# Kernel optimization log

Measured on AMD Instinct MI355X. Metric: run time of the kernel, lower is better.

The kernel has to match this reference:

```python
import jax, jax.numpy as jnp
from jax import lax
import numpy as np

B, C, H, W, D = 8, 128, 96, 96, 4  # D must equal 64//16 = 4 (one UAG per depth slice)


def setup_inputs() -> dict:
    key = jax.random.key(0)
    ks = jax.random.split(key, 9)
    s = 0.5 / np.sqrt(C)  # keep the recurrence numerically stable
    def w(k):
        return jax.random.normal(k, (D, C, C), jnp.float32) * s
    def b(k):
        return jax.random.normal(k, (D, C), jnp.float32) * 0.01
    return {
        "x": jax.random.normal(ks[0], (B, C, H, W, D), jnp.float32),
        "W1": w(ks[1]), "b1": b(ks[2]),  # conv1 per-dag weights/bias (kernel_size=1 -> [C,C])
        "W2": w(ks[3]), "b2": b(ks[4]),  # conv2
        "W4": w(ks[5]), "b4": b(ks[6]),  # conv4
        "W5": w(ks[7]), "b5": b(ks[8]),  # conv5
    }


def _dag(xs, w1, bb1, w2, bb2, w4, bb4, w5, bb5):
    # xs: [B,C,H,W]; one UAG_RNN_4Neigh forward.
    def lin(w, bb, v):  # 1x1 Conv1d == channel matmul; v: [B,C,L]
        return jnp.einsum('oc,bcl->bol', w, v) + bb[None, :, None]

    # --- row recurrence (top -> bottom); row 0 passes through unchanged ---
    def row_step(prev, row):
        new = jax.nn.relu(lin(w1, bb1, row) + lin(w2, bb2, prev))
        return new, new

    row0 = xs[:, :, 0, :]                       # [B,C,W]
    rows = jnp.moveaxis(xs[:, :, 1:, :], 2, 0)  # [H-1,B,C,W]
    _, out_rows = lax.scan(row_step, row0, rows)
    hs = jnp.concatenate([row0[None], out_rows], axis=0)  # [H,B,C,W]
    hs = jnp.moveaxis(hs, 0, 2)                            # [B,C,H,W]

    # --- col recurrence (left -> right); col 0 gets relu only ---
    def col_step(prev, col):
        new = jax.nn.relu(lin(w4, bb4, col) + lin(w5, bb5, prev))
        return new, new

    col0 = jax.nn.relu(hs[:, :, :, 0])           # [B,C,H]
    cols = jnp.moveaxis(hs[:, :, :, 1:], 3, 0)   # [W-1,B,C,H]
    _, out_cols = lax.scan(col_step, col0, cols)
    hse = jnp.concatenate([col0[None], out_cols], axis=0)  # [W,B,C,H]
    return jnp.moveaxis(hse, 0, 3)                           # [B,C,H,W]


def reference(x, W1, b1, W2, b2, W4, b4, W5, b5):
    # vmap over the D=4 depth slices, each with its own dag parameters
    hid = jax.vmap(_dag, in_axes=(-1, 0, 0, 0, 0, 0, 0, 0, 0), out_axes=-1)(
        x, W1, b1, W2, b2, W4, b4, W5, b5)
    return x + hid
```

## Files before the change

kernel.cpp:

```cpp
#include <hip/hip_runtime.h>


typedef short bf16x8 __attribute__((ext_vector_type(8)));
typedef short short4v __attribute__((ext_vector_type(4)));
typedef float f32x4 __attribute__((ext_vector_type(4)));

__device__ __forceinline__ unsigned short f2bf(float f) {
  unsigned int u = __builtin_bit_cast(unsigned int, f);
  u = (u + 0x7FFFu + ((u >> 16) & 1u)) >> 16;
  return (unsigned short)u;
}
__device__ __forceinline__ float bf2f(unsigned short h) {
  unsigned int u = ((unsigned int)h) << 16;
  return __builtin_bit_cast(float, u);
}

#define LDS_BARRIER() asm volatile("s_waitcnt lgkmcnt(0)\n\ts_barrier" ::: "memory")

__global__ __launch_bounds__(256) void prep_kernel(
    const float* __restrict__ W1, const float* __restrict__ b1,
    const float* __restrict__ W2, const float* __restrict__ b2,
    const float* __restrict__ W4, const float* __restrict__ b4,
    const float* __restrict__ W5, const float* __restrict__ b5,
    unsigned short* __restrict__ Wb, float* __restrict__ bs12,
    float* __restrict__ bs45) {
  int gid = blockIdx.x * 256 + threadIdx.x;
  if (gid < 4 * 65536) {
    int m = gid >> 16;
    int r = gid & 65535;
    const float* src = (m == 0) ? W1 : (m == 1) ? W2 : (m == 2) ? W4 : W5;
    Wb[m * 65536 + r] = f2bf(src[r]);
  } else if (gid < 4 * 65536 + 512) {
    int r = gid - 4 * 65536;
    bs12[r] = b1[r] + b2[r];
  } else if (gid < 4 * 65536 + 1024) {
    int r = gid - 4 * 65536 - 512;
    bs45[r] = b4[r] + b5[r];
  }
}

__global__ __launch_bounds__(256) void transpose_kernel(
    const float* __restrict__ x, unsigned short* __restrict__ xT) {
  __shared__ unsigned short tile[128 * 208];
  int bid = blockIdx.x;
  int half = bid & 1;
  int rest = bid >> 1;
  int h = rest % 96;
  int b = rest / 96;
  int wd0 = half * 192;
  int tid = threadIdx.x;
#pragma unroll
  for (int it = 0; it < 12; ++it) {
    int cid = it * 256 + tid;
    int c = cid / 24;
    int k = cid % 24;
    const float* xp = x + ((size_t)(b * 128 + c) * 96 + h) * 384 + wd0 + k * 8;
    float4 v0 = *(const float4*)xp;
    float4 v1 = *(const float4*)(xp + 4);
    bf16x8 pk;
    pk[0] = (short)f2bf(v0.x); pk[1] = (short)f2bf(v0.y);
    pk[2] = (short)f2bf(v0.z); pk[3] = (short)f2bf(v0.w);
    pk[4] = (short)f2bf(v1.x); pk[5] = (short)f2bf(v1.y);
    pk[6] = (short)f2bf(v1.z); pk[7] = (short)f2bf(v1.w);
    int ks = k ^ ((c >> 3) & 7);
    *(bf16x8*)&tile[c * 208 + ks * 8] = pk;
  }
  __syncthreads();
#pragma unroll
  for (int it = 0; it < 12; ++it) {
    int sid = it * 256 + tid;
    int wdl = sid >> 4;
    int cc = sid & 15;
    int c0 = cc * 8;
    int k = wdl >> 3, off = wdl & 7;
    bf16x8 pk;
#pragma unroll
    for (int j = 0; j < 8; ++j) {
      int c = c0 + j;
      int ks = k ^ ((c >> 3) & 7);
      pk[j] = (short)tile[c * 208 + ks * 8 + off];
    }
    int wdg = wd0 + wdl;
    int d = wdg & 3, w = wdg >> 2;
    *(bf16x8*)(xT + ((((size_t)(b * 4 + d) * 96 + h) * 96 + w) * 128 + c0)) = pk;
  }
}

__global__ __launch_bounds__(256) void row_kernel(
    const unsigned short* __restrict__ xT, unsigned short* __restrict__ hs,
    const unsigned short* __restrict__ Wb, const float* __restrict__ bs12) {
  int bid = blockIdx.x;
  int wt = bid % 6;
  int bd = bid / 6;
  int d = bd & 3;
  int w0 = wt * 16;
  int tid = threadIdx.x;
  int lane = tid & 63;
  int wave = tid >> 6;
  int quad = lane >> 4;
  int n = lane & 15;

  __shared__ unsigned short prevs[2][16 * 136];

  const unsigned short* w1p = Wb + d * 16384;
  const unsigned short* w2p = Wb + 65536 + d * 16384;

  bf16x8 A1[2][4], A2[2][4];
#pragma unroll
  for (int mi = 0; mi < 2; ++mi) {
    int c = (wave * 2 + mi) * 16 + n;
#pragma unroll
    for (int kt = 0; kt < 4; ++kt) {
      int k0 = kt * 32 + quad * 8;
      A1[mi][kt] = *(const bf16x8*)(w1p + c * 128 + k0);
      A2[mi][kt] = *(const bf16x8*)(w2p + c * 128 + k0);
    }
  }
  f32x4 bias[2];
#pragma unroll
  for (int mi = 0; mi < 2; ++mi)
#pragma unroll
    for (int r = 0; r < 4; ++r)
      bias[mi][r] = bs12[d * 128 + (wave * 2 + mi) * 16 + quad * 4 + r];

  size_t bd9216 = (size_t)bd * 9216;

  {
    int wl = tid >> 4;
    int c8 = (tid & 15) * 8;
    bf16x8 v = *(const bf16x8*)(xT + (bd9216 + (size_t)(w0 + wl)) * 128 + c8);
    *(bf16x8*)&prevs[0][wl * 136 + c8] = v;
    *(bf16x8*)(hs + (bd9216 + (size_t)(w0 + wl)) * 128 + c8) = v;
  }

  bf16x8 Bt[4], Bn[4], Bf[4];
  {
    const unsigned short* p1 = xT + (bd9216 + (size_t)1 * 96 + w0 + n) * 128;
    const unsigned short* p2 = xT + (bd9216 + (size_t)2 * 96 + w0 + n) * 128;
    const unsigned short* p3 = xT + (bd9216 + (size_t)3 * 96 + w0 + n) * 128;
#pragma unroll
    for (int kt = 0; kt < 4; ++kt) {
      int k0 = kt * 32 + quad * 8;
      Bt[kt] = *(const bf16x8*)(p1 + k0);
      Bn[kt] = *(const bf16x8*)(p2 + k0);
      Bf[kt] = *(const bf16x8*)(p3 + k0);
    }
  }
  f32x4 accA[2] = {bias[0], bias[1]};
#pragma unroll
  for (int kt = 0; kt < 4; ++kt) {
    accA[0] = __builtin_amdgcn_mfma_f32_16x16x32_bf16(A1[0][kt], Bt[kt], accA[0], 0, 0, 0);
    accA[1] = __builtin_amdgcn_mfma_f32_16x16x32_bf16(A1[1][kt], Bt[kt], accA[1], 0, 0, 0);
  }

  for (int h = 1; h < 96; ++h) {
    LDS_BARRIER();
    const unsigned short* pr = &prevs[(h - 1) & 1][n * 136];
    bf16x8 Bp[4];
#pragma unroll
    for (int kt = 0; kt < 4; ++kt)
      Bp[kt] = *(const bf16x8*)(pr + kt * 32 + quad * 8);
    f32x4 acc0 = accA[0], acc1 = accA[1];
#pragma unroll
    for (int kt = 0; kt < 4; ++kt) {
      acc0 = __builtin_amdgcn_mfma_f32_16x16x32_bf16(A2[0][kt], Bp[kt], acc0, 0, 0, 0);
      acc1 = __builtin_amdgcn_mfma_f32_16x16x32_bf16(A2[1][kt], Bp[kt], acc1, 0, 0, 0);
    }
    unsigned short* pw = &prevs[h & 1][n * 136];
    unsigned short* hrow = hs + (bd9216 + (size_t)h * 96 + w0 + n) * 128;
    short4v pk0, pk1;
#pragma unroll
    for (int r = 0; r < 4; ++r) {
      float v = acc0[r]; v = v > 0.f ? v : 0.f; pk0[r] = (short)f2bf(v);
      float u = acc1[r]; u = u > 0.f ? u : 0.f; pk1[r] = (short)f2bf(u);
    }
    int co0 = (wave * 2 + 0) * 16 + quad * 4;
    int co1 = (wave * 2 + 1) * 16 + quad * 4;
    *(short4v*)(pw + co0) = pk0;
    *(short4v*)(pw + co1) = pk1;
    *(short4v*)(hrow + co0) = pk0;
    *(short4v*)(hrow + co1) = pk1;
    accA[0] = bias[0]; accA[1] = bias[1];
#pragma unroll
    for (int kt = 0; kt < 4; ++kt) {
      accA[0] = __builtin_amdgcn_mfma_f32_16x16x32_bf16(A1[0][kt], Bn[kt], accA[0], 0, 0, 0);
      accA[1] = __builtin_amdgcn_mfma_f32_16x16x32_bf16(A1[1][kt], Bn[kt], accA[1], 0, 0, 0);
    }
    int hp = (h + 3 <= 95) ? h + 3 : 95;
    const unsigned short* pf = xT + (bd9216 + (size_t)hp * 96 + w0 + n) * 128;
#pragma unroll
    for (int kt = 0; kt < 4; ++kt) {
      Bn[kt] = Bf[kt];
      Bf[kt] = *(const bf16x8*)(pf + kt * 32 + quad * 8);
    }
  }
}

__global__ __launch_bounds__(256) void col_kernel(
    const unsigned short* __restrict__ hs, unsigned short* __restrict__ hid,
    const unsigned short* __restrict__ Wb, const float* __restrict__ bs45) {
  int bid = blockIdx.x;
  int ht = bid % 6;
  int bd = bid / 6;
  int d = bd & 3;
  int h0 = ht * 16;
  int tid = threadIdx.x;
  int lane = tid & 63;
  int wave = tid >> 6;
  int quad = lane >> 4;
  int n = lane & 15;

  __shared__ unsigned short prevs[2][16 * 136];

  const unsigned short* w4p = Wb + 2 * 65536 + d * 16384;
  const unsigned short* w5p = Wb + 3 * 65536 + d * 16384;

  bf16x8 A4[2][4], A5[2][4];
#pragma unroll
  for (int mi = 0; mi < 2; ++mi) {
    int c = (wave * 2 + mi) * 16 + n;
#pragma unroll
    for (int kt = 0; kt < 4; ++kt) {
      int k0 = kt * 32 + quad * 8;
      A4[mi][kt] = *(const bf16x8*)(w4p + c * 128 + k0);
      A5[mi][kt] = *(const bf16x8*)(w5p + c * 128 + k0);
    }
  }
  f32x4 bias[2];
#pragma unroll
  for (int mi = 0; mi < 2; ++mi)
#pragma unroll
    for (int r = 0; r < 4; ++r)
      bias[mi][r] = bs45[d * 128 + (wave * 2 + mi) * 16 + quad * 4 + r];

  size_t bd9216 = (size_t)bd * 9216;

  {
    int hl = tid >> 4;
    int c8 = (tid & 15) * 8;
    size_t base = (bd9216 + (size_t)(h0 + hl) * 96) * 128 + c8;
    bf16x8 v = *(const bf16x8*)(hs + base);
#pragma unroll
    for (int j = 0; j < 8; ++j) {
      unsigned short uv = (unsigned short)v[j];
      if (uv & 0x8000u) v[j] = 0;
    }
    *(bf16x8*)&prevs[0][hl * 136 + c8] = v;
    *(bf16x8*)(hid + base) = v;
  }

  bf16x8 Bt[4], Bn[4], Bf[4];
  {
    const unsigned short* p1 = hs + (bd9216 + (size_t)(h0 + n) * 96 + 1) * 128;
    const unsigned short* p2 = hs + (bd9216 + (size_t)(h0 + n) * 96 + 2) * 128;
    const unsigned short* p3 = hs + (bd9216 + (size_t)(h0 + n) * 96 + 3) * 128;
#pragma unroll
    for (int kt = 0; kt < 4; ++kt) {
      int k0 = kt * 32 + quad * 8;
      Bt[kt] = *(const bf16x8*)(p1 + k0);
      Bn[kt] = *(const bf16x8*)(p2 + k0);
      Bf[kt] = *(const bf16x8*)(p3 + k0);
    }
  }
  f32x4 accA[2] = {bias[0], bias[1]};
#pragma unroll
  for (int kt = 0; kt < 4; ++kt) {
    accA[0] = __builtin_amdgcn_mfma_f32_16x16x32_bf16(A4[0][kt], Bt[kt], accA[0], 0, 0, 0);
    accA[1] = __builtin_amdgcn_mfma_f32_16x16x32_bf16(A4[1][kt], Bt[kt], accA[1], 0, 0, 0);
  }

  for (int w = 1; w < 96; ++w) {
    LDS_BARRIER();
    const unsigned short* pr = &prevs[(w - 1) & 1][n * 136];
    bf16x8 Bp[4];
#pragma unroll
    for (int kt = 0; kt < 4; ++kt)
      Bp[kt] = *(const bf16x8*)(pr + kt * 32 + quad * 8);
    f32x4 acc0 = accA[0], acc1 = accA[1];
#pragma unroll
    for (int kt = 0; kt < 4; ++kt) {
      acc0 = __builtin_amdgcn_mfma_f32_16x16x32_bf16(A5[0][kt], Bp[kt], acc0, 0, 0, 0);
      acc1 = __builtin_amdgcn_mfma_f32_16x16x32_bf16(A5[1][kt], Bp[kt], acc1, 0, 0, 0);
    }
    unsigned short* pw = &prevs[w & 1][n * 136];
    unsigned short* orow = hid + (bd9216 + (size_t)(h0 + n) * 96 + w) * 128;
    short4v pk0, pk1;
#pragma unroll
    for (int r = 0; r < 4; ++r) {
      float v = acc0[r]; v = v > 0.f ? v : 0.f; pk0[r] = (short)f2bf(v);
      float u = acc1[r]; u = u > 0.f ? u : 0.f; pk1[r] = (short)f2bf(u);
    }
    int co0 = (wave * 2 + 0) * 16 + quad * 4;
    int co1 = (wave * 2 + 1) * 16 + quad * 4;
    *(short4v*)(pw + co0) = pk0;
    *(short4v*)(pw + co1) = pk1;
    *(short4v*)(orow + co0) = pk0;
    *(short4v*)(orow + co1) = pk1;
    accA[0] = bias[0]; accA[1] = bias[1];
#pragma unroll
    for (int kt = 0; kt < 4; ++kt) {
      accA[0] = __builtin_amdgcn_mfma_f32_16x16x32_bf16(A4[0][kt], Bn[kt], accA[0], 0, 0, 0);
      accA[1] = __builtin_amdgcn_mfma_f32_16x16x32_bf16(A4[1][kt], Bn[kt], accA[1], 0, 0, 0);
    }
    int wp = (w + 3 <= 95) ? w + 3 : 95;
    const unsigned short* pf = hs + (bd9216 + (size_t)(h0 + n) * 96 + wp) * 128;
#pragma unroll
    for (int kt = 0; kt < 4; ++kt) {
      Bn[kt] = Bf[kt];
      Bf[kt] = *(const bf16x8*)(pf + kt * 32 + quad * 8);
    }
  }
}

__global__ __launch_bounds__(256) void out_kernel(
    const float* __restrict__ x, const unsigned short* __restrict__ hid,
    float* __restrict__ out) {
  __shared__ unsigned short tile[128 * 208];
  int bid = blockIdx.x;
  int half = bid & 1;
  int rest = bid >> 1;
  int h = rest % 96;
  int b = rest / 96;
  int wd0 = half * 192;
  int tid = threadIdx.x;
#pragma unroll
  for (int it = 0; it < 12; ++it) {
    int gid = it * 256 + tid;
    int wdl = gid >> 4;
    int cc = gid & 15;
    int c0 = cc * 8;
    int wdg = wd0 + wdl;
    int d = wdg & 3, w = wdg >> 2;
    bf16x8 v = *(const bf16x8*)(hid + ((((size_t)(b * 4 + d) * 96 + h) * 96 + w) * 128 + c0));
    int k = wdl >> 3, off = wdl & 7;
#pragma unroll
    for (int j = 0; j < 8; ++j) {
      int c = c0 + j;
      int ks = k ^ ((c >> 3) & 7);
      tile[c * 208 + ks * 8 + off] = (unsigned short)v[j];
    }
  }
  __syncthreads();
#pragma unroll
  for (int it = 0; it < 12; ++it) {
    int sid = it * 256 + tid;
    int c = sid / 24;
    int k = sid % 24;
    int ks = k ^ ((c >> 3) & 7);
    bf16x8 pk = *(const bf16x8*)&tile[c * 208 + ks * 8];
    size_t o = ((size_t)(b * 128 + c) * 96 + h) * 384 + wd0 + k * 8;
    float4 a0 = *(const float4*)(x + o);
    float4 a1 = *(const float4*)(x + o + 4);
    float4 r0, r1;
    r0.x = a0.x + bf2f((unsigned short)pk[0]);
    r0.y = a0.y + bf2f((unsigned short)pk[1]);
    r0.z = a0.z + bf2f((unsigned short)pk[2]);
    r0.w = a0.w + bf2f((unsigned short)pk[3]);
    r1.x = a1.x + bf2f((unsigned short)pk[4]);
    r1.y = a1.y + bf2f((unsigned short)pk[5]);
    r1.z = a1.z + bf2f((unsigned short)pk[6]);
    r1.w = a1.w + bf2f((unsigned short)pk[7]);
    *(float4*)(out + o) = r0;
    *(float4*)(out + o + 4) = r1;
  }
}

extern "C" void kernel_launch(void* const* d_in, const int* in_sizes, int n_in,
                              void* d_out, int out_size, void* d_ws, size_t ws_size,
                              hipStream_t stream) {
  (void)in_sizes; (void)n_in; (void)out_size; (void)ws_size;
  const float* x  = (const float*)d_in[0];
  const float* W1 = (const float*)d_in[1];
  const float* b1 = (const float*)d_in[2];
  const float* W2 = (const float*)d_in[3];
  const float* b2 = (const float*)d_in[4];
  const float* W4 = (const float*)d_in[5];
  const float* b4 = (const float*)d_in[6];
  const float* W5 = (const float*)d_in[7];
  const float* b5 = (const float*)d_in[8];
  float* out = (float*)d_out;

  char* ws = (char*)d_ws;
  unsigned short* Wb   = (unsigned short*)(ws);
  float* bs12          = (float*)(ws + 524288);
  float* bs45          = (float*)(ws + 526336);
  unsigned short* hs   = (unsigned short*)(ws + 528384);
  unsigned short* xT   = (unsigned short*)(ws + 76025856);
  unsigned short* hid  = xT;

  prep_kernel<<<(4 * 65536 + 1024 + 255) / 256, 256, 0, stream>>>(
      W1, b1, W2, b2, W4, b4, W5, b5, Wb, bs12, bs45);
  transpose_kernel<<<8 * 96 * 2, 256, 0, stream>>>(x, xT);
  row_kernel<<<192, 256, 0, stream>>>(xT, hs, Wb, bs12);
  col_kernel<<<192, 256, 0, stream>>>(hs, hid, Wb, bs45);
  out_kernel<<<8 * 96 * 2, 256, 0, stream>>>(x, hid, out);
}
```

Before: 493.6 us.

## Keep recurrence state in registers with a permuted channel layout in single-wave blocks

Channel order in the weights and activations is permuted so that each MFMA output fragment, once packed to bf16, is already the B operand for the next step. This lets a single wave per block hold all 128 output channels and carry the recurrent state in registers, removing the LDS round trip and barrier each step. The row and column scans now overwrite one in-place activation buffer, and bf16 conversion uses v_cvt_pk_bf16_f32 with two-step software pipelining. The cost is far fewer waves per CU (192 single-wave blocks), heavy VGPR pressure from 64 weight fragments, and a longer serial MFMA chain per wave.

```diff
diff --git a/kernel.cpp b/kernel.cpp
--- a/kernel.cpp
+++ b/kernel.cpp
@@ -2,8 +2,8 @@
 
 
 typedef short bf16x8 __attribute__((ext_vector_type(8)));
-typedef short short4v __attribute__((ext_vector_type(4)));
 typedef float f32x4 __attribute__((ext_vector_type(4)));
+typedef unsigned int uint4v __attribute__((ext_vector_type(4)));
 
 __device__ __forceinline__ unsigned short f2bf(float f) {
   unsigned int u = __builtin_bit_cast(unsigned int, f);
@@ -15,7 +15,10 @@
   return __builtin_bit_cast(float, u);
 }
 
-#define LDS_BARRIER() asm volatile("s_waitcnt lgkmcnt(0)\n\ts_barrier" ::: "memory")
+__device__ __forceinline__ int sigma_k(int kap) {
+  int kt = kap >> 5, q = (kap >> 3) & 3, j = kap & 7;
+  return kt * 32 + ((j >> 2) << 4) + q * 4 + (j & 3);
+}
 
 __global__ __launch_bounds__(256) void prep_kernel(
     const float* __restrict__ W1, const float* __restrict__ b1,
@@ -28,8 +31,10 @@
   if (gid < 4 * 65536) {
     int m = gid >> 16;
     int r = gid & 65535;
+    int kap = r & 127;
+    int c = sigma_k(kap);
     const float* src = (m == 0) ? W1 : (m == 1) ? W2 : (m == 2) ? W4 : W5;
-    Wb[m * 65536 + r] = f2bf(src[r]);
+    Wb[m * 65536 + r] = f2bf(src[(r >> 7) * 128 + c]);
   } else if (gid < 4 * 65536 + 512) {
     int r = gid - 4 * 65536;
     bs12[r] = b1[r] + b2[r];
@@ -40,7 +45,7 @@
 }
 
 __global__ __launch_bounds__(256) void transpose_kernel(
-    const float* __restrict__ x, unsigned short* __restrict__ xT) {
+    const float* __restrict__ x, unsigned short* __restrict__ act) {
   __shared__ unsigned short tile[128 * 208];
   int bid = blockIdx.x;
   int half = bid & 1;
@@ -71,249 +76,223 @@
     int sid = it * 256 + tid;
     int wdl = sid >> 4;
     int cc = sid & 15;
-    int c0 = cc * 8;
     int k = wdl >> 3, off = wdl & 7;
+    int ktq = cc >> 2, qq = cc & 3;
     bf16x8 pk;
 #pragma unroll
     for (int j = 0; j < 8; ++j) {
-      int c = c0 + j;
+      int c = ktq * 32 + ((j >> 2) << 4) + qq * 4 + (j & 3);
       int ks = k ^ ((c >> 3) & 7);
       pk[j] = (short)tile[c * 208 + ks * 8 + off];
     }
     int wdg = wd0 + wdl;
     int d = wdg & 3, w = wdg >> 2;
-    *(bf16x8*)(xT + ((((size_t)(b * 4 + d) * 96 + h) * 96 + w) * 128 + c0)) = pk;
-  }
-}
-
-__global__ __launch_bounds__(256) void row_kernel(
-    const unsigned short* __restrict__ xT, unsigned short* __restrict__ hs,
-    const unsigned short* __restrict__ Wb, const float* __restrict__ bs12) {
+    *(bf16x8*)(act + ((((size_t)(b * 4 + d) * 96 + h) * 96 + w) * 128 + cc * 8)) = pk;
+  }
+}
+
+#define SCAN_STEP(CUR, NXT, BN, PF)                                            \
+  do {                                                                         \
+    _Pragma("unroll") for (int kt = 0; kt < 4; ++kt)                           \
+      _Pragma("unroll") for (int mi = 0; mi < 8; ++mi)                         \
+        CUR[mi] = __builtin_amdgcn_mfma_f32_16x16x32_bf16(A2[mi][kt], Bp[kt],  \
+                                                          CUR[mi], 0, 0, 0);   \
+    _Pragma("unroll") for (int kt = 0; kt < 4; ++kt) {                         \
+      unsigned int u0, u1, u2, u3;                                             \
+      float a0 = fmaxf(CUR[2 * kt][0], 0.f);                                   \
+      float a1 = fmaxf(CUR[2 * kt][1], 0.f);                                   \
+      float a2 = fmaxf(CUR[2 * kt][2], 0.f);                                   \
+      float a3 = fmaxf(CUR[2 * kt][3], 0.f);                                   \
+      float c0 = fmaxf(CUR[2 * kt + 1][0], 0.f);                               \
+      float c1 = fmaxf(CUR[2 * kt + 1][1], 0.f);                               \
+      float c2 = fmaxf(CUR[2 * kt + 1][2], 0.f);                               \
+      float c3 = fmaxf(CUR[2 * kt + 1][3], 0.f);                               \
+      asm("v_cvt_pk_bf16_f32 %0, %1, %2" : "=v"(u0) : "v"(a0), "v"(a1));       \
+      asm("v_cvt_pk_bf16_f32 %0, %1, %2" : "=v"(u1) : "v"(a2), "v"(a3));       \
+      asm("v_cvt_pk_bf16_f32 %0, %1, %2" : "=v"(u2) : "v"(c0), "v"(c1));       \
+      asm("v_cvt_pk_bf16_f32 %0, %1, %2" : "=v"(u3) : "v"(c2), "v"(c3));       \
+      uint4v uu;                                                               \
+      uu[0] = u0; uu[1] = u1; uu[2] = u2; uu[3] = u3;                          \
+      Bp[kt] = __builtin_bit_cast(bf16x8, uu);                                 \
+      *(bf16x8*)(outrow + kt * 32) = Bp[kt];                                   \
+    }                                                                          \
+    _Pragma("unroll") for (int mi = 0; mi < 8; ++mi)                           \
+      NXT[mi] = __builtin_amdgcn_mfma_f32_16x16x32_bf16(A1[mi][0], BN[0],      \
+                                                        bias[mi], 0, 0, 0);    \
+    _Pragma("unroll") for (int kt = 1; kt < 4; ++kt)                           \
+      _Pragma("unroll") for (int mi = 0; mi < 8; ++mi)                         \
+        NXT[mi] = __builtin_amdgcn_mfma_f32_16x16x32_bf16(A1[mi][kt], BN[kt],  \
+                                                          NXT[mi], 0, 0, 0);   \
+    _Pragma("unroll") for (int kt = 0; kt < 4; ++kt)                           \
+      BN[kt] = *(const bf16x8*)(PF + kt * 32);                                 \
+    outrow += OUT_STRIDE;                                                      \
+  } while (0)
+
+__global__ __launch_bounds__(64, 1) void row_kernel(
+    unsigned short* act, const unsigned short* __restrict__ Wb,
+    const float* __restrict__ bs12) {
   int bid = blockIdx.x;
   int wt = bid % 6;
   int bd = bid / 6;
   int d = bd & 3;
   int w0 = wt * 16;
-  int tid = threadIdx.x;
-  int lane = tid & 63;
-  int wave = tid >> 6;
-  int quad = lane >> 4;
+  int lane = threadIdx.x & 63;
+  int q = lane >> 4;
   int n = lane & 15;
-
-  __shared__ unsigned short prevs[2][16 * 136];
 
   const unsigned short* w1p = Wb + d * 16384;
   const unsigned short* w2p = Wb + 65536 + d * 16384;
 
-  bf16x8 A1[2][4], A2[2][4];
-#pragma unroll
-  for (int mi = 0; mi < 2; ++mi) {
-    int c = (wave * 2 + mi) * 16 + n;
+  bf16x8 A1[8][4], A2[8][4];
+#pragma unroll
+  for (int mi = 0; mi < 8; ++mi) {
+    int c = mi * 16 + n;
 #pragma unroll
     for (int kt = 0; kt < 4; ++kt) {
-      int k0 = kt * 32 + quad * 8;
+      int k0 = kt * 32 + q * 8;
       A1[mi][kt] = *(const bf16x8*)(w1p + c * 128 + k0);
       A2[mi][kt] = *(const bf16x8*)(w2p + c * 128 + k0);
     }
   }
-  f32x4 bias[2];
-#pragma unroll
-  for (int mi = 0; mi < 2; ++mi)
+  f32x4 bias[8];
+#pragma unroll
+  for (int mi = 0; mi < 8; ++mi)
 #pragma unroll
     for (int r = 0; r < 4; ++r)
-      bias[mi][r] = bs12[d * 128 + (wave * 2 + mi) * 16 + quad * 4 + r];
-
-  size_t bd9216 = (size_t)bd * 9216;
-
+      bias[mi][r] = bs12[d * 128 + mi * 16 + q * 4 + r];
+
+  size_t base = ((size_t)bd * 9216 + (size_t)(w0 + n)) * 128 + q * 8;
+  const unsigned short* xrow = act + base;
+  unsigned short* outrow = act + base + 12288;
+  const int OUT_STRIDE = 12288;
+
+  bf16x8 Bp[4], Bn_[4], Bf_[4];
+#pragma unroll
+  for (int kt = 0; kt < 4; ++kt)
+    Bp[kt] = *(const bf16x8*)(xrow + kt * 32);
+
+  f32x4 accA_[8], accB_[8];
+#pragma unroll
+  for (int kt = 0; kt < 4; ++kt)
+    Bn_[kt] = *(const bf16x8*)(xrow + 12288 + kt * 32);
+#pragma unroll
+  for (int mi = 0; mi < 8; ++mi)
+    accA_[mi] = __builtin_amdgcn_mfma_f32_16x16x32_bf16(A1[mi][0], Bn_[0],
+                                                        bias[mi], 0, 0, 0);
+#pragma unroll
+  for (int kt = 1; kt < 4; ++kt)
+#pragma unroll
+    for (int mi = 0; mi < 8; ++mi)
+      accA_[mi] = __builtin_amdgcn_mfma_f32_16x16x32_bf16(A1[mi][kt], Bn_[kt],
+                                                          accA_[mi], 0, 0, 0);
+#pragma unroll
+  for (int kt = 0; kt < 4; ++kt) {
+    Bn_[kt] = *(const bf16x8*)(xrow + 2 * 12288 + kt * 32);
+    Bf_[kt] = *(const bf16x8*)(xrow + 3 * 12288 + kt * 32);
+  }
+
+#pragma unroll 1
+  for (int h = 1; h <= 93; h += 2) {
+    const unsigned short* pf1 =
+        xrow + (size_t)(h + 3 <= 95 ? h + 3 : 95) * 12288;
+    SCAN_STEP(accA_, accB_, Bn_, pf1);
+    const unsigned short* pf2 =
+        xrow + (size_t)(h + 4 <= 95 ? h + 4 : 95) * 12288;
+    SCAN_STEP(accB_, accA_, Bf_, pf2);
+  }
   {
-    int wl = tid >> 4;
-    int c8 = (tid & 15) * 8;
-    bf16x8 v = *(const bf16x8*)(xT + (bd9216 + (size_t)(w0 + wl)) * 128 + c8);
-    *(bf16x8*)&prevs[0][wl * 136 + c8] = v;
-    *(bf16x8*)(hs + (bd9216 + (size_t)(w0 + wl)) * 128 + c8) = v;
-  }
-
-  bf16x8 Bt[4], Bn[4], Bf[4];
-  {
-    const unsigned short* p1 = xT + (bd9216 + (size_t)1 * 96 + w0 + n) * 128;
-    const unsigned short* p2 = xT + (bd9216 + (size_t)2 * 96 + w0 + n) * 128;
-    const unsigned short* p3 = xT + (bd9216 + (size_t)3 * 96 + w0 + n) * 128;
-#pragma unroll
-    for (int kt = 0; kt < 4; ++kt) {
-      int k0 = kt * 32 + quad * 8;
-      Bt[kt] = *(const bf16x8*)(p1 + k0);
-      Bn[kt] = *(const bf16x8*)(p2 + k0);
-      Bf[kt] = *(const bf16x8*)(p3 + k0);
-    }
-  }
-  f32x4 accA[2] = {bias[0], bias[1]};
-#pragma unroll
-  for (int kt = 0; kt < 4; ++kt) {
-    accA[0] = __builtin_amdgcn_mfma_f32_16x16x32_bf16(A1[0][kt], Bt[kt], accA[0], 0, 0, 0);
-    accA[1] = __builtin_amdgcn_mfma_f32_16x16x32_bf16(A1[1][kt], Bt[kt], accA[1], 0, 0, 0);
-  }
-
-  for (int h = 1; h < 96; ++h) {
-    LDS_BARRIER();
-    const unsigned short* pr = &prevs[(h - 1) & 1][n * 136];
-    bf16x8 Bp[4];
-#pragma unroll
-    for (int kt = 0; kt < 4; ++kt)
-      Bp[kt] = *(const bf16x8*)(pr + kt * 32 + quad * 8);
-    f32x4 acc0 = accA[0], acc1 = accA[1];
-#pragma unroll
-    for (int kt = 0; kt < 4; ++kt) {
-      acc0 = __builtin_amdgcn_mfma_f32_16x16x32_bf16(A2[0][kt], Bp[kt], acc0, 0, 0, 0);
-      acc1 = __builtin_amdgcn_mfma_f32_16x16x32_bf16(A2[1][kt], Bp[kt], acc1, 0, 0, 0);
-    }
-    unsigned short* pw = &prevs[h & 1][n * 136];
-    unsigned short* hrow = hs + (bd9216 + (size_t)h * 96 + w0 + n) * 128;
-    short4v pk0, pk1;
-#pragma unroll
-    for (int r = 0; r < 4; ++r) {
-      float v = acc0[r]; v = v > 0.f ? v : 0.f; pk0[r] = (short)f2bf(v);
-      float u = acc1[r]; u = u > 0.f ? u : 0.f; pk1[r] = (short)f2bf(u);
-    }
-    int co0 = (wave * 2 + 0) * 16 + quad * 4;
-    int co1 = (wave * 2 + 1) * 16 + quad * 4;
-    *(short4v*)(pw + co0) = pk0;
-    *(short4v*)(pw + co1) = pk1;
-    *(short4v*)(hrow + co0) = pk0;
-    *(short4v*)(hrow + co1) = pk1;
-    accA[0] = bias[0]; accA[1] = bias[1];
-#pragma unroll
-    for (int kt = 0; kt < 4; ++kt) {
-      accA[0] = __builtin_amdgcn_mfma_f32_16x16x32_bf16(A1[0][kt], Bn[kt], accA[0], 0, 0, 0);
-      accA[1] = __builtin_amdgcn_mfma_f32_16x16x32_bf16(A1[1][kt], Bn[kt], accA[1], 0, 0, 0);
-    }
-    int hp = (h + 3 <= 95) ? h + 3 : 95;
-    const unsigned short* pf = xT + (bd9216 + (size_t)hp * 96 + w0 + n) * 128;
-#pragma unroll
-    for (int kt = 0; kt < 4; ++kt) {
-      Bn[kt] = Bf[kt];
-      Bf[kt] = *(const bf16x8*)(pf + kt * 32 + quad * 8);
-    }
-  }
-}
-
-__global__ __launch_bounds__(256) void col_kernel(
-    const unsigned short* __restrict__ hs, unsigned short* __restrict__ hid,
-    const unsigned short* __restrict__ Wb, const float* __restrict__ bs45) {
+    const unsigned short* pf3 = xrow + (size_t)95 * 12288;
+    SCAN_STEP(accA_, accB_, Bn_, pf3);
+  }
+}
+
+__global__ __launch_bounds__(64, 1) void col_kernel(
+    unsigned short* act, const unsigned short* __restrict__ Wb,
+    const float* __restrict__ bs45) {
   int bid = blockIdx.x;
   int ht = bid % 6;
   int bd = bid / 6;
   int d = bd & 3;
   int h0 = ht * 16;
-  int tid = threadIdx.x;
-  int lane = tid & 63;
-  int wave = tid >> 6;
-  int quad = lane >> 4;
+  int lane = threadIdx.x & 63;
+  int q = lane >> 4;
   int n = lane & 15;
-
-  __shared__ unsigned short prevs[2][16 * 136];
 
   const unsigned short* w4p = Wb + 2 * 65536 + d * 16384;
   const unsigned short* w5p = Wb + 3 * 65536 + d * 16384;
 
-  bf16x8 A4[2][4], A5[2][4];
-#pragma unroll
-  for (int mi = 0; mi < 2; ++mi) {
-    int c = (wave * 2 + mi) * 16 + n;
+  bf16x8 A1[8][4], A2[8][4];
+#pragma unroll
+  for (int mi = 0; mi < 8; ++mi) {
+    int c = mi * 16 + n;
 #pragma unroll
     for (int kt = 0; kt < 4; ++kt) {
-      int k0 = kt * 32 + quad * 8;
-      A4[mi][kt] = *(const bf16x8*)(w4p + c * 128 + k0);
-      A5[mi][kt] = *(const bf16x8*)(w5p + c * 128 + k0);
-    }
-  }
-  f32x4 bias[2];
-#pragma unroll
-  for (int mi = 0; mi < 2; ++mi)
+      int k0 = kt * 32 + q * 8;
+      A1[mi][kt] = *(const bf16x8*)(w4p + c * 128 + k0);
+      A2[mi][kt] = *(const bf16x8*)(w5p + c * 128 + k0);
+    }
+  }
+  f32x4 bias[8];
+#pragma unroll
+  for (int mi = 0; mi < 8; ++mi)
 #pragma unroll
     for (int r = 0; r < 4; ++r)
-      bias[mi][r] = bs45[d * 128 + (wave * 2 + mi) * 16 + quad * 4 + r];
-
-  size_t bd9216 = (size_t)bd * 9216;
-
-  {
-    int hl = tid >> 4;
-    int c8 = (tid & 15) * 8;
-    size_t base = (bd9216 + (size_t)(h0 + hl) * 96) * 128 + c8;
-    bf16x8 v = *(const bf16x8*)(hs + base);
+      bias[mi][r] = bs45[d * 128 + mi * 16 + q * 4 + r];
+
+  size_t base = ((size_t)bd * 9216 + (size_t)(h0 + n) * 96) * 128 + q * 8;
+  const unsigned short* ccol = act + base;
+  unsigned short* outrow = act + base;
+  const int OUT_STRIDE = 128;
+
+  bf16x8 Bp[4], Bn_[4], Bf_[4];
+#pragma unroll
+  for (int kt = 0; kt < 4; ++kt) {
+    bf16x8 v = *(const bf16x8*)(ccol + kt * 32);
 #pragma unroll
     for (int j = 0; j < 8; ++j) {
       unsigned short uv = (unsigned short)v[j];
       if (uv & 0x8000u) v[j] = 0;
     }
-    *(bf16x8*)&prevs[0][hl * 136 + c8] = v;
-    *(bf16x8*)(hid + base) = v;
-  }
-
-  bf16x8 Bt[4], Bn[4], Bf[4];
+    Bp[kt] = v;
+    *(bf16x8*)(outrow + kt * 32) = v;
+  }
+  outrow += 128;
+
+  f32x4 accA_[8], accB_[8];
+#pragma unroll
+  for (int kt = 0; kt < 4; ++kt)
+    Bn_[kt] = *(const bf16x8*)(ccol + 128 + kt * 32);
+#pragma unroll
+  for (int mi = 0; mi < 8; ++mi)
+    accA_[mi] = __builtin_amdgcn_mfma_f32_16x16x32_bf16(A1[mi][0], Bn_[0],
+                                                        bias[mi], 0, 0, 0);
+#pragma unroll
+  for (int kt = 1; kt < 4; ++kt)
+#pragma unroll
+    for (int mi = 0; mi < 8; ++mi)
+      accA_[mi] = __builtin_amdgcn_mfma_f32_16x16x32_bf16(A1[mi][kt], Bn_[kt],
+                                                          accA_[mi], 0, 0, 0);
+#pragma unroll
+  for (int kt = 0; kt < 4; ++kt) {
+    Bn_[kt] = *(const bf16x8*)(ccol + 2 * 128 + kt * 32);
+    Bf_[kt] = *(const bf16x8*)(ccol + 3 * 128 + kt * 32);
+  }
+
+#pragma unroll 1
+  for (int w = 1; w <= 93; w += 2) {
+    const unsigned short* pf1 = ccol + (size_t)(w + 3 <= 95 ? w + 3 : 95) * 128;
+    SCAN_STEP(accA_, accB_, Bn_, pf1);
+    const unsigned short* pf2 = ccol + (size_t)(w + 4 <= 95 ? w + 4 : 95) * 128;
+    SCAN_STEP(accB_, accA_, Bf_, pf2);
+  }
   {
-    const unsigned short* p1 = hs + (bd9216 + (size_t)(h0 + n) * 96 + 1) * 128;
-    const unsigned short* p2 = hs + (bd9216 + (size_t)(h0 + n) * 96 + 2) * 128;
-    const unsigned short* p3 = hs + (bd9216 + (size_t)(h0 + n) * 96 + 3) * 128;
-#pragma unroll
-    for (int kt = 0; kt < 4; ++kt) {
-      int k0 = kt * 32 + quad * 8;
-      Bt[kt] = *(const bf16x8*)(p1 + k0);
-      Bn[kt] = *(const bf16x8*)(p2 + k0);
-      Bf[kt] = *(const bf16x8*)(p3 + k0);
-    }
-  }
-  f32x4 accA[2] = {bias[0], bias[1]};
-#pragma unroll
-  for (int kt = 0; kt < 4; ++kt) {
-    accA[0] = __builtin_amdgcn_mfma_f32_16x16x32_bf16(A4[0][kt], Bt[kt], accA[0], 0, 0, 0);
-    accA[1] = __builtin_amdgcn_mfma_f32_16x16x32_bf16(A4[1][kt], Bt[kt], accA[1], 0, 0, 0);
-  }
-
-  for (int w = 1; w < 96; ++w) {
-    LDS_BARRIER();
-    const unsigned short* pr = &prevs[(w - 1) & 1][n * 136];
-    bf16x8 Bp[4];
-#pragma unroll
-    for (int kt = 0; kt < 4; ++kt)
-      Bp[kt] = *(const bf16x8*)(pr + kt * 32 + quad * 8);
-    f32x4 acc0 = accA[0], acc1 = accA[1];
-#pragma unroll
-    for (int kt = 0; kt < 4; ++kt) {
-      acc0 = __builtin_amdgcn_mfma_f32_16x16x32_bf16(A5[0][kt], Bp[kt], acc0, 0, 0, 0);
-      acc1 = __builtin_amdgcn_mfma_f32_16x16x32_bf16(A5[1][kt], Bp[kt], acc1, 0, 0, 0);
-    }
-    unsigned short* pw = &prevs[w & 1][n * 136];
-    unsigned short* orow = hid + (bd9216 + (size_t)(h0 + n) * 96 + w) * 128;
-    short4v pk0, pk1;
-#pragma unroll
-    for (int r = 0; r < 4; ++r) {
-      float v = acc0[r]; v = v > 0.f ? v : 0.f; pk0[r] = (short)f2bf(v);
-      float u = acc1[r]; u = u > 0.f ? u : 0.f; pk1[r] = (short)f2bf(u);
-    }
-    int co0 = (wave * 2 + 0) * 16 + quad * 4;
-    int co1 = (wave * 2 + 1) * 16 + quad * 4;
-    *(short4v*)(pw + co0) = pk0;
-    *(short4v*)(pw + co1) = pk1;
-    *(short4v*)(orow + co0) = pk0;
-    *(short4v*)(orow + co1) = pk1;
-    accA[0] = bias[0]; accA[1] = bias[1];
-#pragma unroll
-    for (int kt = 0; kt < 4; ++kt) {
-      accA[0] = __builtin_amdgcn_mfma_f32_16x16x32_bf16(A4[0][kt], Bn[kt], accA[0], 0, 0, 0);
-      accA[1] = __builtin_amdgcn_mfma_f32_16x16x32_bf16(A4[1][kt], Bn[kt], accA[1], 0, 0, 0);
-    }
-    int wp = (w + 3 <= 95) ? w + 3 : 95;
-    const unsigned short* pf = hs + (bd9216 + (size_t)(h0 + n) * 96 + wp) * 128;
-#pragma unroll
-    for (int kt = 0; kt < 4; ++kt) {
-      Bn[kt] = Bf[kt];
-      Bf[kt] = *(const bf16x8*)(pf + kt * 32 + quad * 8);
-    }
+    const unsigned short* pf3 = ccol + (size_t)95 * 128;
+    SCAN_STEP(accA_, accB_, Bn_, pf3);
   }
 }
 
 __global__ __launch_bounds__(256) void out_kernel(
-    const float* __restrict__ x, const unsigned short* __restrict__ hid,
+    const float* __restrict__ x, const unsigned short* __restrict__ act,
     float* __restrict__ out) {
   __shared__ unsigned short tile[128 * 208];
   int bid = blockIdx.x;
@@ -328,14 +307,15 @@
     int gid = it * 256 + tid;
     int wdl = gid >> 4;
     int cc = gid & 15;
-    int c0 = cc * 8;
     int wdg = wd0 + wdl;
     int d = wdg & 3, w = wdg >> 2;
-    bf16x8 v = *(const bf16x8*)(hid + ((((size_t)(b * 4 + d) * 96 + h) * 96 + w) * 128 + c0));
+    bf16x8 v = *(const bf16x8*)(
+        act + ((((size_t)(b * 4 + d) * 96 + h) * 96 + w) * 128 + cc * 8));
     int k = wdl >> 3, off = wdl & 7;
+    int ktq = cc >> 2, qq = cc & 3;
 #pragma unroll
     for (int j = 0; j < 8; ++j) {
-      int c = c0 + j;
+      int c = ktq * 32 + ((j >> 2) << 4) + qq * 4 + (j & 3);
       int ks = k ^ ((c >> 3) & 7);
       tile[c * 208 + ks * 8 + off] = (unsigned short)v[j];
     }
@@ -366,8 +346,8 @@
 }
 
 extern "C" void kernel_launch(void* const* d_in, const int* in_sizes, int n_in,
-                              void* d_out, int out_size, void* d_ws, size_t ws_size,
-                              hipStream_t stream) {
+                              void* d_out, int out_size, void* d_ws,
+                              size_t ws_size, hipStream_t stream) {
   (void)in_sizes; (void)n_in; (void)out_size; (void)ws_size;
   const float* x  = (const float*)d_in[0];
   const float* W1 = (const float*)d_in[1];
@@ -381,17 +361,15 @@
   float* out = (float*)d_out;
 
   char* ws = (char*)d_ws;
-  unsigned short* Wb   = (unsigned short*)(ws);
-  float* bs12          = (float*)(ws + 524288);
-  float* bs45          = (float*)(ws + 526336);
-  unsigned short* hs   = (unsigned short*)(ws + 528384);
-  unsigned short* xT   = (unsigned short*)(ws + 76025856);
-  unsigned short* hid  = xT;
+  unsigned short* Wb  = (unsigned short*)(ws);
+  float* bs12         = (float*)(ws + 524288);
+  float* bs45         = (float*)(ws + 526336);
+  unsigned short* act = (unsigned short*)(ws + 528384);
 
   prep_kernel<<<(4 * 65536 + 1024 + 255) / 256, 256, 0, stream>>>(
       W1, b1, W2, b2, W4, b4, W5, b5, Wb, bs12, bs45);
-  transpose_kernel<<<8 * 96 * 2, 256, 0, stream>>>(x, xT);
-  row_kernel<<<192, 256, 0, stream>>>(xT, hs, Wb, bs12);
-  col_kernel<<<192, 256, 0, stream>>>(hs, hid, Wb, bs45);
-  out_kernel<<<8 * 96 * 2, 256, 0, stream>>>(x, hid, out);
-}
+  transpose_kernel<<<8 * 96 * 2, 256, 0, stream>>>(x, act);
+  row_kernel<<<192, 64, 0, stream>>>(act, Wb, bs12);
+  col_kernel<<<192, 64, 0, stream>>>(act, Wb, bs45);
+  out_kernel<<<8 * 96 * 2, 256, 0, stream>>>(x, act, out);
+}
```

Result: slower. 518.7 us (+5.1%).
